# Kernel tuning notes

Measured on AMD Instinct MI355X. Metric: run time of the kernel, lower is better.

The kernel has to match this reference:

```python
import jax, jax.numpy as jnp
import numpy as np

NUM_ENT = 40000
NUM_REL = 20


def _rgcn_layer(x, src, dst, et, comp, basis, root, bias, act):
    # Basis decomposition: W_r = sum_b comp[r, b] * basis[b]  -> [R, in, out]
    W = jnp.einsum('rb,bio->rio', comp, basis)
    # Per-(dst, relation) sum of source features: equivalent to per-edge
    # transform W_{et[e]} @ x[src[e]] then scatter-sum, but transforms after
    # aggregation (linear, so identical math) to avoid an [E, in, out] gather.
    seg = dst * NUM_REL + et                       # combined segment id
    S = jax.ops.segment_sum(x[src], seg, num_segments=NUM_ENT * NUM_REL)
    S = S.reshape(NUM_ENT, NUM_REL, x.shape[1])    # [N, R, in]
    agg = jnp.einsum('nri,rio->no', S, W)          # [N, out]
    # mean aggregation over ALL incoming edges (PyG RGCNConv aggr='mean')
    deg = jax.ops.segment_sum(jnp.ones(src.shape[0], x.dtype), dst,
                              num_segments=NUM_ENT)
    agg = agg / jnp.clip(deg, 1.0)[:, None]
    out = agg + x @ root + bias
    return jnp.tanh(out) if act else out


def setup_inputs() -> dict:
    key = jax.random.key(0)
    ks = jax.random.split(key, 16)
    E = 640000
    d = 128
    B = 8
    s = 0.05
    return {
        'edge_index': jax.random.randint(ks[0], (2, E), 0, NUM_ENT),
        'edge_type': jax.random.randint(ks[1], (E,), 0, NUM_REL),
        'init_embed': jax.random.normal(ks[2], (NUM_ENT, d), jnp.float32) * s,
        'init_rel': jax.random.normal(ks[3], (NUM_REL * 2, d), jnp.float32) * s,
        'w_rel': jax.random.normal(ks[4], (d, d), jnp.float32) * s,
        'comp1': jax.random.normal(ks[5], (NUM_REL, B), jnp.float32) * s,
        'basis1': jax.random.normal(ks[6], (B, d, d), jnp.float32) * s,
        'root1': jax.random.normal(ks[7], (d, d), jnp.float32) * s,
        'bias1': jax.random.normal(ks[8], (d,), jnp.float32) * s,
        'comp2': jax.random.normal(ks[9], (NUM_REL, B), jnp.float32) * s,
        'basis2': jax.random.normal(ks[10], (B, d, d), jnp.float32) * s,
        'root2': jax.random.normal(ks[11], (d, d), jnp.float32) * s,
        'bias2': jax.random.normal(ks[12], (d,), jnp.float32) * s,
    }


def reference(edge_index, edge_type, init_embed, init_rel, w_rel,
              comp1, basis1, root1, bias1, comp2, basis2, root2, bias2):
    src, dst = edge_index[0], edge_index[1]
    x = init_embed
    # layer 1: init_dim -> gcn_dim, act=tanh (gcn_layer=2)
    x = _rgcn_layer(x, src, dst, edge_type, comp1, basis1, root1, bias1, True)
    # dropout is identity at inference
    # layer 2: embed_dim -> embed_dim, act=None
    x = _rgcn_layer(x, src, dst, edge_type, comp2, basis2, root2, bias2, False)
    r = init_rel @ w_rel
    return (x, r)
```

## Files before the change

### kernel.cpp

```cpp
#include <hip/hip_runtime.h>
#include <hip/hip_bf16.h>

#define NENT 40000
#define NREL 20
#define DIM 128
#define NBASIS 8
#define TILE 16
#define PKCAP 512
#define SCANBLK 157

typedef __attribute__((ext_vector_type(8))) short sh8;
typedef __attribute__((ext_vector_type(4))) float fx4;

__device__ __forceinline__ short f2bf(float f) {
    union { __hip_bfloat16 h; short s; } u;
    u.h = __float2bfloat16(f);
    return u.s;
}

__global__ void k_tobf(const float* __restrict__ x, ushort* __restrict__ xb, int nelem) {
    int i = (blockIdx.x * 256 + threadIdx.x) * 4;
    if (i >= nelem) return;
    float4 v = *(const float4*)(x + i);
    ushort4 o;
    o.x = (ushort)f2bf(v.x); o.y = (ushort)f2bf(v.y);
    o.z = (ushort)f2bf(v.z); o.w = (ushort)f2bf(v.w);
    *(ushort4*)(xb + i) = o;
}

__global__ void k_wfrag9(const float* __restrict__ basis, const float* __restrict__ root,
                         short* __restrict__ Wfb) {
    int t = blockIdx.x * 256 + threadIdx.x;
    if (t >= 9 * 16384) return;
    int ks = t / 16384;
    int rem = t & 16383;
    int i = rem >> 7, o = rem & 127;
    float v = (ks < 8) ? basis[ks * 16384 + i * 128 + o] : root[i * 128 + o];
    int c = o >> 4, l15 = o & 15;
    int kk = i >> 5, lhi = (i >> 3) & 3, e = i & 7;
    int lane = l15 + lhi * 16;
    Wfb[(size_t)ks * 16384 + (size_t)(((c * 4 + kk) * 64 + lane) << 3) + e] = f2bf(v);
}

__global__ void k_hist(const int* __restrict__ dst, int E, int* __restrict__ hist) {
    int e = blockIdx.x * 256 + threadIdx.x;
    if (e < E) atomicAdd(&hist[dst[e]], 1);
}

__global__ void k_scan1(const int* __restrict__ hist, int* __restrict__ offs,
                        int* __restrict__ bsum) {
    __shared__ int ps[256];
    int t = threadIdx.x;
    int i = blockIdx.x * 256 + t;
    int v = (i < NENT) ? hist[i] : 0;
    ps[t] = v;
    __syncthreads();
    for (int off = 1; off < 256; off <<= 1) {
        int u = (t >= off) ? ps[t - off] : 0;
        __syncthreads();
        ps[t] += u;
        __syncthreads();
    }
    if (i < NENT) offs[i] = ps[t] - v;
    if (t == 255) bsum[blockIdx.x] = ps[255];
}

__global__ void k_scan2(int* __restrict__ bsum) {
    __shared__ int ps[256];
    int t = threadIdx.x;
    int v = (t < SCANBLK) ? bsum[t] : 0;
    ps[t] = v;
    __syncthreads();
    for (int off = 1; off < 256; off <<= 1) {
        int u = (t >= off) ? ps[t - off] : 0;
        __syncthreads();
        ps[t] += u;
        __syncthreads();
    }
    if (t < SCANBLK) bsum[t] = ps[t] - v;
}

__global__ void k_scan3(int* __restrict__ offs, int* __restrict__ cursor,
                        const int* __restrict__ bsum, int E) {
    int i = blockIdx.x * 256 + threadIdx.x;
    if (i < NENT) {
        int o = offs[i] + bsum[blockIdx.x];
        offs[i] = o;
        cursor[i] = o;
    }
    if (i == 0) offs[NENT] = E;
}

__global__ void k_scatter(const int* __restrict__ et, const int* __restrict__ srcA,
                          const int* __restrict__ dstA, int E,
                          int* __restrict__ cursor, unsigned* __restrict__ packed) {
    int e = blockIdx.x * 256 + threadIdx.x;
    if (e >= E) return;
    int pos = atomicAdd(&cursor[dstA[e]], 1);
    packed[pos] = (unsigned)srcA[e] | ((unsigned)et[e] << 16);
}

#define GLDS(dst, voff, sbase)                                             \
    asm volatile("global_load_dword %0, %1, %2"                            \
                 : "=v"(dst) : "v"(voff), "s"(sbase))

#define WAITV(N)                                                           \
    do {                                                                   \
        asm volatile("s_waitcnt vmcnt(" #N ")" ::: "memory");              \
        __builtin_amdgcn_sched_barrier(0);                                 \
    } while (0)

__global__ __launch_bounds__(512) void k_fused(
    const ushort* __restrict__ xb, const unsigned* __restrict__ packed,
    const int* __restrict__ offs, const float* __restrict__ comp,
    const short* __restrict__ Wfb, const float* __restrict__ bias,
    ushort* __restrict__ outbf, float* __restrict__ outf, int act) {
    __shared__ __align__(16) ushort Gl[TILE * 1024];
    __shared__ __align__(16) unsigned pkl[PKCAP];

    int t = threadIdx.x;
    int lane = t & 63, wid = t >> 6;
    unsigned lane4 = (unsigned)(lane * 4);

    int tile0 = blockIdx.x * TILE;
    int base = offs[tile0];
    int totE = offs[tile0 + TILE] - base;
    for (int i = t; i < totE && i < PKCAP; i += 512) pkl[i] = packed[base + i];
    __syncthreads();

    bool fast = (totE <= PKCAP);
    for (int sub = 0; sub < 2; ++sub) {
        int row = wid * 2 + sub;
        int n = tile0 + row;
        int begg = offs[n];
        int cnt = offs[n + 1] - begg;
        int begl = begg - base;

        float a0[NBASIS], a1[NBASIS];
#pragma unroll
        for (int b = 0; b < NBASIS; ++b) { a0[b] = 0.f; a1[b] = 0.f; }

        if (cnt > 0 && fast) {
            int sbA[8], seA[8], sbB[8], seB[8];
            unsigned rA[8], rB[8];

            auto ldp = [&](int i0, int (&sb)[8], int (&se)[8]) {
#pragma unroll
                for (int u = 0; u < 8; ++u) {
                    int i = i0 + u;
                    int li = begl + (i < cnt ? i : 0);
                    unsigned p = __builtin_amdgcn_readfirstlane(pkl[li]);
                    sb[u] = (int)(p & 0xFFFFu) * 256;
                    se[u] = (int)(p >> 16);
                }
            };
            auto issue = [&](const int (&sb)[8], unsigned (&r)[8]) {
#pragma unroll
                for (int u = 0; u < 8; ++u) {
                    const char* bp = (const char*)xb + sb[u];
                    GLDS(r[u], lane4, bp);
                }
            };
            auto proc = [&](int i0, const int (&se)[8], const unsigned (&r)[8]) {
#pragma unroll
                for (int u = 0; u < 8; ++u) {
                    if (i0 + u < cnt) {
                        const float4* cp = (const float4*)(comp + se[u] * NBASIS);
                        float4 cwa = cp[0];
                        float4 cwb = cp[1];
                        float xlo = __uint_as_float(r[u] << 16);
                        float xhi = __uint_as_float(r[u] & 0xFFFF0000u);
                        a0[0] += cwa.x * xlo; a1[0] += cwa.x * xhi;
                        a0[1] += cwa.y * xlo; a1[1] += cwa.y * xhi;
                        a0[2] += cwa.z * xlo; a1[2] += cwa.z * xhi;
                        a0[3] += cwa.w * xlo; a1[3] += cwa.w * xhi;
                        a0[4] += cwb.x * xlo; a1[4] += cwb.x * xhi;
                        a0[5] += cwb.y * xlo; a1[5] += cwb.y * xhi;
                        a0[6] += cwb.z * xlo; a1[6] += cwb.z * xhi;
                        a0[7] += cwb.w * xlo; a1[7] += cwb.w * xhi;
                    }
                }
            };

            ldp(0, sbA, seA); issue(sbA, rA);
            int i0 = 0;
            while (i0 < cnt) {
                ldp(i0 + 8, sbB, seB); issue(sbB, rB);
                WAITV(8);
                proc(i0, seA, rA);
                i0 += 8;
                if (i0 >= cnt) break;
                ldp(i0 + 8, sbA, seA); issue(sbA, rA);
                WAITV(8);
                proc(i0, seB, rB);
                i0 += 8;
            }
            asm volatile("s_waitcnt vmcnt(0)" ::: "memory");
            __builtin_amdgcn_sched_barrier(0);
        } else if (cnt > 0) {
            const unsigned* xrow = (const unsigned*)xb + lane;
            unsigned pA = packed[begg], pB = 0, rA = xrow[(size_t)(pA & 0xFFFFu) * 64];
            if (cnt > 1) pB = packed[begg + 1];
            for (int i = 0; i < cnt; ++i) {
                unsigned pC = (i + 2 < cnt) ? packed[begg + i + 2] : 0u;
                unsigned rB = xrow[(size_t)(pB & 0xFFFFu) * 64];
                float xlo = __uint_as_float(rA << 16);
                float xhi = __uint_as_float(rA & 0xFFFF0000u);
                int et = pA >> 16;
                const float4* cp = (const float4*)(comp + et * NBASIS);
                float4 cwa = cp[0];
                float4 cwb = cp[1];
                a0[0] += cwa.x * xlo; a1[0] += cwa.x * xhi;
                a0[1] += cwa.y * xlo; a1[1] += cwa.y * xhi;
                a0[2] += cwa.z * xlo; a1[2] += cwa.z * xhi;
                a0[3] += cwa.w * xlo; a1[3] += cwa.w * xhi;
                a0[4] += cwb.x * xlo; a1[4] += cwb.x * xhi;
                a0[5] += cwb.y * xlo; a1[5] += cwb.y * xhi;
                a0[6] += cwb.z * xlo; a1[6] += cwb.z * xhi;
                a0[7] += cwb.w * xlo; a1[7] += cwb.w * xhi;
                pA = pB; pB = pC; rA = rB;
            }
        }

        float inv = 1.f / (float)(cnt < 1 ? 1 : cnt);
#pragma unroll
        for (int b = 0; b < NBASIS; ++b) {
            unsigned lo = (unsigned)(ushort)f2bf(a0[b] * inv);
            unsigned hi = (unsigned)(ushort)f2bf(a1[b] * inv);
            unsigned byteoff = (unsigned)(row * 2048 + b * 256 + lane * 4);
            byteoff ^= (unsigned)((row & 7) << 4);
            *(unsigned*)((char*)Gl + byteoff) = lo | (hi << 16);
        }
    }
    __syncthreads();

    int l15 = lane & 15, lhi = lane >> 4;
    int c = wid;

    fx4 acc0 = (fx4){0.f, 0.f, 0.f, 0.f};

    const sh8* W8 = (const sh8*)Wfb;

#pragma unroll
    for (int ks = 0; ks < 9; ++ks) {
        sh8 a0f[4];
        if (ks < 8) {
#pragma unroll
            for (int kk = 0; kk < 4; ++kk) {
                int ar0 = l15;
                unsigned bo0 = (unsigned)(ar0 * 2048 + ks * 256 + kk * 64 + lhi * 16);
                bo0 ^= (unsigned)((ar0 & 7) << 4);
                a0f[kk] = *(const sh8*)((const char*)Gl + bo0);
            }
        } else {
#pragma unroll
            for (int kk = 0; kk < 4; ++kk) {
                a0f[kk] = *(const sh8*)(xb + (size_t)(tile0 + l15) * 128 + lhi * 8 + kk * 32);
            }
        }
#pragma unroll
        for (int kk = 0; kk < 4; ++kk) {
            sh8 b = W8[(size_t)ks * 2048 + (size_t)((c * 4 + kk) * 64 + lane)];
            acc0 = __builtin_amdgcn_mfma_f32_16x16x32_bf16(a0f[kk], b, acc0, 0, 0, 0);
        }
    }

    int col = c * 16 + l15;
    float bv = bias[col];
    int orow0 = tile0 + lhi * 4;
#pragma unroll
    for (int j = 0; j < 4; ++j) {
        float v = acc0[j] + bv;
        if (act) {
            v = tanhf(v);
            outbf[(size_t)(orow0 + j) * 128 + col] = (ushort)f2bf(v);
        } else {
            outf[(size_t)(orow0 + j) * 128 + col] = v;
        }
    }
}

__global__ void k_rel(const float* __restrict__ rel, const float* __restrict__ wrel,
                      float* __restrict__ out, int nrows) {
    int idx = blockIdx.x * 256 + threadIdx.x;
    if (idx >= nrows * DIM) return;
    int j = idx >> 7, o = idx & 127;
    float s = 0.f;
    for (int i = 0; i < DIM; ++i) s += rel[j * DIM + i] * wrel[i * DIM + o];
    out[idx] = s;
}

extern "C" void kernel_launch(void* const* d_in, const int* in_sizes, int n_in,
                              void* d_out, int out_size, void* d_ws, size_t ws_size,
                              hipStream_t stream) {
    const int* edge_index = (const int*)d_in[0];
    const int* edge_type  = (const int*)d_in[1];
    const float* init_embed = (const float*)d_in[2];
    const float* init_rel   = (const float*)d_in[3];
    const float* w_rel      = (const float*)d_in[4];
    const float* comp1  = (const float*)d_in[5];
    const float* basis1 = (const float*)d_in[6];
    const float* root1  = (const float*)d_in[7];
    const float* bias1  = (const float*)d_in[8];
    const float* comp2  = (const float*)d_in[9];
    const float* basis2 = (const float*)d_in[10];
    const float* root2  = (const float*)d_in[11];
    const float* bias2  = (const float*)d_in[12];

    int E = in_sizes[1];
    const int* src = edge_index;
    const int* dst = edge_index + E;
    int relrows = in_sizes[3] / DIM;

    short* Wfb1 = (short*)d_ws;
    short* Wfb2 = Wfb1 + (size_t)9 * 16384;
    ushort* xb  = (ushort*)(Wfb2 + (size_t)9 * 16384);
    ushort* hb  = xb + (size_t)NENT * DIM;
    int* hist   = (int*)(hb + (size_t)NENT * DIM);
    int* offs   = hist + 40004;
    int* cursor = offs + 40004;
    int* bsum   = cursor + 40004;
    unsigned* packed = (unsigned*)(bsum + 160);

    float* outx = (float*)d_out;
    float* outr = outx + (size_t)NENT * DIM;

    hipMemsetAsync(hist, 0, NENT * sizeof(int), stream);

    k_tobf<<<(NENT * DIM / 4 + 255) / 256, 256, 0, stream>>>(init_embed, xb, NENT * DIM);
    k_wfrag9<<<(9 * 16384 + 255) / 256, 256, 0, stream>>>(basis1, root1, Wfb1);
    k_wfrag9<<<(9 * 16384 + 255) / 256, 256, 0, stream>>>(basis2, root2, Wfb2);
    k_hist<<<(E + 255) / 256, 256, 0, stream>>>(dst, E, hist);
    k_scan1<<<SCANBLK, 256, 0, stream>>>(hist, offs, bsum);
    k_scan2<<<1, 256, 0, stream>>>(bsum);
    k_scan3<<<SCANBLK, 256, 0, stream>>>(offs, cursor, bsum, E);
    k_scatter<<<(E + 255) / 256, 256, 0, stream>>>(edge_type, src, dst, E, cursor, packed);

    k_fused<<<NENT / TILE, 512, 0, stream>>>(xb, packed, offs, comp1, Wfb1, bias1,
                                             hb, outx, 1);
    k_fused<<<NENT / TILE, 512, 0, stream>>>(hb, packed, offs, comp2, Wfb2, bias2,
                                             hb, outx, 0);

    k_rel<<<(relrows * DIM + 255) / 256, 256, 0, stream>>>(init_rel, w_rel, outr, relrows);
}
```

Measured before the change: 228.1 us.

## Merge prep kernels into one launch and use packed float2 FMAs in aggregation

Folds the bf16 conversion, both weight-fragment packings, the degree histogram and the relation matmul into a single k_prep launch, with each job assigned its own range of block indices. This removes several kernel launches and the gaps between them. It also rewrites the per-edge accumulation in k_fused as 2-wide float vector FMAs so the compiler can emit packed FP32 instructions. The block ranges are hardcoded for NENT=40000 and E=640000, so other sizes would break.

```diff
diff --git a/kernel.cpp b/kernel.cpp
--- a/kernel.cpp
+++ b/kernel.cpp
@@ -11,6 +11,7 @@
 
 typedef __attribute__((ext_vector_type(8))) short sh8;
 typedef __attribute__((ext_vector_type(4))) float fx4;
+typedef __attribute__((ext_vector_type(2))) float f32x2;
 
 __device__ __forceinline__ short f2bf(float f) {
     union { __hip_bfloat16 h; short s; } u;
@@ -18,9 +19,9 @@
     return u.s;
 }
 
-__global__ void k_tobf(const float* __restrict__ x, ushort* __restrict__ xb, int nelem) {
-    int i = (blockIdx.x * 256 + threadIdx.x) * 4;
-    if (i >= nelem) return;
+__device__ __forceinline__ void d_tobf(int b, int t, const float* __restrict__ x,
+                                       ushort* __restrict__ xb) {
+    int i = (b * 256 + t) * 4;
     float4 v = *(const float4*)(x + i);
     ushort4 o;
     o.x = (ushort)f2bf(v.x); o.y = (ushort)f2bf(v.y);
@@ -28,10 +29,10 @@
     *(ushort4*)(xb + i) = o;
 }
 
-__global__ void k_wfrag9(const float* __restrict__ basis, const float* __restrict__ root,
-                         short* __restrict__ Wfb) {
-    int t = blockIdx.x * 256 + threadIdx.x;
-    if (t >= 9 * 16384) return;
+__device__ __forceinline__ void d_wfrag9(int b, int tt, const float* __restrict__ basis,
+                                         const float* __restrict__ root,
+                                         short* __restrict__ Wfb) {
+    int t = b * 256 + tt;
     int ks = t / 16384;
     int rem = t & 16383;
     int i = rem >> 7, o = rem & 127;
@@ -42,9 +43,33 @@
     Wfb[(size_t)ks * 16384 + (size_t)(((c * 4 + kk) * 64 + lane) << 3) + e] = f2bf(v);
 }
 
-__global__ void k_hist(const int* __restrict__ dst, int E, int* __restrict__ hist) {
-    int e = blockIdx.x * 256 + threadIdx.x;
-    if (e < E) atomicAdd(&hist[dst[e]], 1);
+__global__ void k_prep(const float* __restrict__ x, ushort* __restrict__ xb,
+                       const float* __restrict__ basis1, const float* __restrict__ root1,
+                       short* __restrict__ Wfb1,
+                       const float* __restrict__ basis2, const float* __restrict__ root2,
+                       short* __restrict__ Wfb2,
+                       const int* __restrict__ dst, int E, int* __restrict__ hist,
+                       const float* __restrict__ rel, const float* __restrict__ wrel,
+                       float* __restrict__ outr, int relrows) {
+    int b = blockIdx.x, t = threadIdx.x;
+    if (b < 5000) {
+        d_tobf(b, t, x, xb);
+    } else if (b < 5576) {
+        d_wfrag9(b - 5000, t, basis1, root1, Wfb1);
+    } else if (b < 6152) {
+        d_wfrag9(b - 5576, t, basis2, root2, Wfb2);
+    } else if (b < 8652) {
+        int e = (b - 6152) * 256 + t;
+        if (e < E) atomicAdd(&hist[dst[e]], 1);
+    } else {
+        int idx = (b - 8652) * 256 + t;
+        if (idx < relrows * DIM) {
+            int j = idx >> 7, o = idx & 127;
+            float s = 0.f;
+            for (int i = 0; i < DIM; ++i) s += rel[j * DIM + i] * wrel[i * DIM + o];
+            outr[idx] = s;
+        }
+    }
 }
 
 __global__ void k_scan1(const int* __restrict__ hist, int* __restrict__ offs,
@@ -110,6 +135,16 @@
         __builtin_amdgcn_sched_barrier(0);                                 \
     } while (0)
 
+#define FMA8(AV, CWA, CWB, XP)                                             \
+    AV[0] += (f32x2){(CWA).x, (CWA).x} * (XP);                             \
+    AV[1] += (f32x2){(CWA).y, (CWA).y} * (XP);                             \
+    AV[2] += (f32x2){(CWA).z, (CWA).z} * (XP);                             \
+    AV[3] += (f32x2){(CWA).w, (CWA).w} * (XP);                             \
+    AV[4] += (f32x2){(CWB).x, (CWB).x} * (XP);                             \
+    AV[5] += (f32x2){(CWB).y, (CWB).y} * (XP);                             \
+    AV[6] += (f32x2){(CWB).z, (CWB).z} * (XP);                             \
+    AV[7] += (f32x2){(CWB).w, (CWB).w} * (XP);
+
 __global__ __launch_bounds__(512) void k_fused(
     const ushort* __restrict__ xb, const unsigned* __restrict__ packed,
     const int* __restrict__ offs, const float* __restrict__ comp,
@@ -136,9 +171,9 @@
         int cnt = offs[n + 1] - begg;
         int begl = begg - base;
 
-        float a0[NBASIS], a1[NBASIS];
-#pragma unroll
-        for (int b = 0; b < NBASIS; ++b) { a0[b] = 0.f; a1[b] = 0.f; }
+        f32x2 av[NBASIS];
+#pragma unroll
+        for (int b = 0; b < NBASIS; ++b) av[b] = (f32x2){0.f, 0.f};
 
         if (cnt > 0 && fast) {
             int sbA[8], seA[8], sbB[8], seB[8];
@@ -168,16 +203,9 @@
                         const float4* cp = (const float4*)(comp + se[u] * NBASIS);
                         float4 cwa = cp[0];
                         float4 cwb = cp[1];
-                        float xlo = __uint_as_float(r[u] << 16);
-                        float xhi = __uint_as_float(r[u] & 0xFFFF0000u);
-                        a0[0] += cwa.x * xlo; a1[0] += cwa.x * xhi;
-                        a0[1] += cwa.y * xlo; a1[1] += cwa.y * xhi;
-                        a0[2] += cwa.z * xlo; a1[2] += cwa.z * xhi;
-                        a0[3] += cwa.w * xlo; a1[3] += cwa.w * xhi;
-                        a0[4] += cwb.x * xlo; a1[4] += cwb.x * xhi;
-                        a0[5] += cwb.y * xlo; a1[5] += cwb.y * xhi;
-                        a0[6] += cwb.z * xlo; a1[6] += cwb.z * xhi;
-                        a0[7] += cwb.w * xlo; a1[7] += cwb.w * xhi;
+                        f32x2 xp = {__uint_as_float(r[u] << 16),
+                                    __uint_as_float(r[u] & 0xFFFF0000u)};
+                        FMA8(av, cwa, cwb, xp)
                     }
                 }
             };
@@ -204,20 +232,13 @@
             for (int i = 0; i < cnt; ++i) {
                 unsigned pC = (i + 2 < cnt) ? packed[begg + i + 2] : 0u;
                 unsigned rB = xrow[(size_t)(pB & 0xFFFFu) * 64];
-                float xlo = __uint_as_float(rA << 16);
-                float xhi = __uint_as_float(rA & 0xFFFF0000u);
                 int et = pA >> 16;
                 const float4* cp = (const float4*)(comp + et * NBASIS);
                 float4 cwa = cp[0];
                 float4 cwb = cp[1];
-                a0[0] += cwa.x * xlo; a1[0] += cwa.x * xhi;
-                a0[1] += cwa.y * xlo; a1[1] += cwa.y * xhi;
-                a0[2] += cwa.z * xlo; a1[2] += cwa.z * xhi;
-                a0[3] += cwa.w * xlo; a1[3] += cwa.w * xhi;
-                a0[4] += cwb.x * xlo; a1[4] += cwb.x * xhi;
-                a0[5] += cwb.y * xlo; a1[5] += cwb.y * xhi;
-                a0[6] += cwb.z * xlo; a1[6] += cwb.z * xhi;
-                a0[7] += cwb.w * xlo; a1[7] += cwb.w * xhi;
+                f32x2 xp = {__uint_as_float(rA << 16),
+                            __uint_as_float(rA & 0xFFFF0000u)};
+                FMA8(av, cwa, cwb, xp)
                 pA = pB; pB = pC; rA = rB;
             }
         }
@@ -225,8 +246,8 @@
         float inv = 1.f / (float)(cnt < 1 ? 1 : cnt);
 #pragma unroll
         for (int b = 0; b < NBASIS; ++b) {
-            unsigned lo = (unsigned)(ushort)f2bf(a0[b] * inv);
-            unsigned hi = (unsigned)(ushort)f2bf(a1[b] * inv);
+            unsigned lo = (unsigned)(ushort)f2bf(av[b][0] * inv);
+            unsigned hi = (unsigned)(ushort)f2bf(av[b][1] * inv);
             unsigned byteoff = (unsigned)(row * 2048 + b * 256 + lane * 4);
             byteoff ^= (unsigned)((row & 7) << 4);
             *(unsigned*)((char*)Gl + byteoff) = lo | (hi << 16);
@@ -278,16 +299,6 @@
             outf[(size_t)(orow0 + j) * 128 + col] = v;
         }
     }
-}
-
-__global__ void k_rel(const float* __restrict__ rel, const float* __restrict__ wrel,
-                      float* __restrict__ out, int nrows) {
-    int idx = blockIdx.x * 256 + threadIdx.x;
-    if (idx >= nrows * DIM) return;
-    int j = idx >> 7, o = idx & 127;
-    float s = 0.f;
-    for (int i = 0; i < DIM; ++i) s += rel[j * DIM + i] * wrel[i * DIM + o];
-    out[idx] = s;
 }
 
 extern "C" void kernel_launch(void* const* d_in, const int* in_sizes, int n_in,
@@ -327,10 +338,10 @@
 
     hipMemsetAsync(hist, 0, NENT * sizeof(int), stream);
 
-    k_tobf<<<(NENT * DIM / 4 + 255) / 256, 256, 0, stream>>>(init_embed, xb, NENT * DIM);
-    k_wfrag9<<<(9 * 16384 + 255) / 256, 256, 0, stream>>>(basis1, root1, Wfb1);
-    k_wfrag9<<<(9 * 16384 + 255) / 256, 256, 0, stream>>>(basis2, root2, Wfb2);
-    k_hist<<<(E + 255) / 256, 256, 0, stream>>>(dst, E, hist);
+    int relblocks = (relrows * DIM + 255) / 256;
+    k_prep<<<8652 + relblocks, 256, 0, stream>>>(
+        init_embed, xb, basis1, root1, Wfb1, basis2, root2, Wfb2,
+        dst, E, hist, init_rel, w_rel, outr, relrows);
     k_scan1<<<SCANBLK, 256, 0, stream>>>(hist, offs, bsum);
     k_scan2<<<1, 256, 0, stream>>>(bsum);
     k_scan3<<<SCANBLK, 256, 0, stream>>>(offs, cursor, bsum, E);
@@ -340,6 +351,4 @@
                                              hb, outx, 1);
     k_fused<<<NENT / TILE, 512, 0, stream>>>(hb, packed, offs, comp2, Wfb2, bias2,
                                              hb, outx, 0);
-
-    k_rel<<<(relrows * DIM + 255) / 256, 256, 0, stream>>>(init_rel, w_rel, outr, relrows);
-}
+}
```

Measured after the change: 220.9 us (median of 2 runs). 3.2% less time.
